# Kernel optimization log

Hardware: AMD Instinct MI355X
Metric: run time of the kernel (lower is better)

Reference implementation:

```python
import jax, jax.numpy as jnp
import numpy as np

N_NODES = 100000
N_EDGES = 3200000


def _spmm(rows, cols, vals, x):
    # out[i] = sum_{e: rows[e]==i} vals[e] * x[cols[e]]
    msgs = vals[:, None] * x[cols]  # [E, F]
    return jax.ops.segment_sum(msgs, rows, num_segments=N_NODES)


def setup_inputs() -> dict:
    key = jax.random.key(0)
    ks = jax.random.split(key, 8)
    x = jax.random.normal(ks[0], (N_NODES, 256), dtype=jnp.float32)
    adj_rows = jax.random.randint(ks[1], (N_EDGES,), 0, N_NODES, dtype=jnp.int32)
    adj_cols = jax.random.randint(ks[2], (N_EDGES,), 0, N_NODES, dtype=jnp.int32)
    adj_vals = jax.random.uniform(ks[3], (N_EDGES,), dtype=jnp.float32)
    W1 = jax.random.normal(ks[4], (256, 128), dtype=jnp.float32) * (1.0 / np.sqrt(256))
    b1 = jnp.zeros((128,), dtype=jnp.float32)
    W2 = jax.random.normal(ks[5], (128, 64), dtype=jnp.float32) * (1.0 / np.sqrt(128))
    b2 = jnp.zeros((64,), dtype=jnp.float32)
    return {"x": x, "adj_rows": adj_rows, "adj_cols": adj_cols, "adj_vals": adj_vals,
            "W1": W1, "b1": b1, "W2": W2, "b2": b2}


def reference(x, adj_rows, adj_cols, adj_vals, W1, b1, W2, b2):
    # Layer 0: spmm -> linear -> relu (dropout inactive in eval)
    h = _spmm(adj_rows, adj_cols, adj_vals, x)
    h = jax.nn.relu(h @ W1 + b1)
    # Layer 1 (last layer): spmm -> linear, no activation
    h = _spmm(adj_rows, adj_cols, adj_vals, h)
    out = h @ W2 + b2
    return out  # squeeze(1) is a no-op for [N, nclass]
```

## Files before the change

### kernel.cpp

```cpp
#include <hip/hip_runtime.h>
#include <hip/hip_fp16.h>


#define RPB 480
#define NB_MAX 1024
#define PCHUNK 8192
#define EPT 32

typedef _Float16 half8 __attribute__((ext_vector_type(8)));
typedef float floatx4 __attribute__((ext_vector_type(4)));

__global__ __launch_bounds__(256) void zero_i32_kernel(int* __restrict__ p, int n) {
    int i = blockIdx.x * 256 + threadIdx.x;
    if (i < n) p[i] = 0;
}

__global__ __launch_bounds__(256) void transpose_w_kernel(const float* __restrict__ W,
                                                          __half* __restrict__ WT,
                                                          int K, int N) {
    int i = blockIdx.x * 256 + threadIdx.x;
    if (i < K * N) {
        int k = i / N, n = i % N;
        WT[n * K + k] = __float2half_rn(W[i]);
    }
}

__global__ __launch_bounds__(256) void bucket_hist_kernel(const int* __restrict__ rows,
                                                          int* __restrict__ gcnt,
                                                          int nE, int nB) {
    __shared__ int hist[NB_MAX];
    const int t = threadIdx.x;
    const int c0 = blockIdx.x * PCHUNK;
    const int c1 = min(c0 + PCHUNK, nE);
    for (int b = t; b < nB; b += 256) hist[b] = 0;
    __syncthreads();
    for (int e = c0 + t; e < c1; e += 256) atomicAdd(&hist[rows[e] / RPB], 1);
    __syncthreads();
    for (int b = t; b < nB; b += 256) {
        int c = hist[b];
        if (c) atomicAdd(&gcnt[b], c);
    }
}

__global__ __launch_bounds__(1024) void bucket_scan_kernel(const int* __restrict__ gcnt,
                                                           int* __restrict__ boff,
                                                           int* __restrict__ gcur,
                                                           int* __restrict__ off,
                                                           int nB, int nN) {
    __shared__ int part[1024];
    int t = threadIdx.x;
    int v = (t < nB) ? gcnt[t] : 0;
    part[t] = v;
    __syncthreads();
    for (int d = 1; d < 1024; d <<= 1) {
        int add = (t >= d) ? part[t - d] : 0;
        __syncthreads();
        part[t] += add;
        __syncthreads();
    }
    if (t < nB) {
        int excl = part[t] - v;
        boff[t] = excl;
        gcur[t] = excl;
    }
    if (t == 1023) {
        boff[nB] = part[1023];
        off[nN] = part[1023];
    }
}

__global__ __launch_bounds__(256) void partition_kernel(const int* __restrict__ rows,
                                                        const int* __restrict__ cols,
                                                        const float* __restrict__ vals,
                                                        int* __restrict__ gcur,
                                                        int2* __restrict__ eb1,
                                                        int nE, int nB) {
    __shared__ int hist[NB_MAX];
    __shared__ int cur[NB_MAX];
    const int t = threadIdx.x;
    const int c0 = blockIdx.x * PCHUNK;
    for (int b = t; b < nB; b += 256) hist[b] = 0;
    __syncthreads();
    int myr[EPT];
#pragma unroll
    for (int j = 0; j < EPT; ++j) {
        int e = c0 + t + 256 * j;
        int r = (e < nE) ? rows[e] : -1;
        myr[j] = r;
        if (r >= 0) atomicAdd(&hist[r / RPB], 1);
    }
    __syncthreads();
    for (int b = t; b < nB; b += 256) {
        int c = hist[b];
        cur[b] = c ? atomicAdd(&gcur[b], c) : 0;
    }
    __syncthreads();
#pragma unroll
    for (int j = 0; j < EPT; ++j) {
        int r = myr[j];
        if (r >= 0) {
            int e = c0 + t + 256 * j;
            int bk = r / RPB;
            int rl = r - bk * RPB;
            int pos = atomicAdd(&cur[bk], 1);
            eb1[pos] = make_int2((cols[e] & 0x1FFFF) | (rl << 17), __float_as_int(vals[e]));
        }
    }
}

__global__ __launch_bounds__(512) void fine_scatter_kernel(const int* __restrict__ boff,
                                                           const int2* __restrict__ eb1,
                                                           int2* __restrict__ eb2,
                                                           int* __restrict__ off,
                                                           int nN) {
    __shared__ int hist[RPB];
    __shared__ int sc[RPB];
    __shared__ int cur[RPB];
    const int b = blockIdx.x;
    const int row0 = b * RPB;
    const int nr = min(RPB, nN - row0);
    const int t = threadIdx.x;
    const int s = boff[b];
    const int e = boff[b + 1];

    if (t < RPB) hist[t] = 0;
    __syncthreads();
    for (int i = s + t; i < e; i += 512)
        atomicAdd(&hist[((unsigned)eb1[i].x) >> 17], 1);
    __syncthreads();

    int myc = (t < RPB) ? hist[t] : 0;
    if (t < RPB) sc[t] = myc;
    __syncthreads();
    for (int d = 1; d < RPB; d <<= 1) {
        int add = (t < RPB && t >= d) ? sc[t - d] : 0;
        __syncthreads();
        if (t < RPB) sc[t] += add;
        __syncthreads();
    }
    if (t < RPB) {
        int excl = s + sc[t] - myc;
        cur[t] = excl;
        if (t < nr) off[row0 + t] = excl;
    }
    __syncthreads();

    for (int i = s + t; i < e; i += 512) {
        int2 ed = eb1[i];
        unsigned x = (unsigned)ed.x;
        int pos = atomicAdd(&cur[x >> 17], 1);
        eb2[pos] = make_int2((int)(x & 0x1FFFF), ed.y);
    }
}

template <int F>
__global__ __launch_bounds__(256) void spmm_csr_kernel(const int* __restrict__ off,
                                                       const int2* __restrict__ eb,
                                                       const __half* __restrict__ Y,
                                                       const float* __restrict__ bias,
                                                       float* __restrict__ out, int nN) {
    int row = blockIdx.x * 4 + (threadIdx.x >> 6);
    if (row >= nN) return;
    int lane = threadIdx.x & 63;
    int s = off[row];
    int e1 = off[row + 1];

    float2 acc;
    if (F == 128) acc = make_float2(bias[lane * 2], bias[lane * 2 + 1]);
    else          acc = make_float2(bias[lane], 0.f);

    for (int base = s; base < e1; base += 64) {
        int n = min(64, e1 - base);
        int2 my = (lane < n) ? eb[base + lane] : make_int2(0, 0);
        int j = 0;
        for (; j + 4 <= n; j += 4) {
            int c0 = __shfl(my.x, j + 0), c1 = __shfl(my.x, j + 1);
            int c2 = __shfl(my.x, j + 2), c3 = __shfl(my.x, j + 3);
            float v0 = __int_as_float(__shfl(my.y, j + 0));
            float v1 = __int_as_float(__shfl(my.y, j + 1));
            float v2 = __int_as_float(__shfl(my.y, j + 2));
            float v3 = __int_as_float(__shfl(my.y, j + 3));
            if (F == 128) {
                float2 y0 = __half22float2(*((const __half2*)(Y + (size_t)c0 * 128) + lane));
                float2 y1 = __half22float2(*((const __half2*)(Y + (size_t)c1 * 128) + lane));
                float2 y2 = __half22float2(*((const __half2*)(Y + (size_t)c2 * 128) + lane));
                float2 y3 = __half22float2(*((const __half2*)(Y + (size_t)c3 * 128) + lane));
                acc.x = fmaf(v0, y0.x, acc.x); acc.y = fmaf(v0, y0.y, acc.y);
                acc.x = fmaf(v1, y1.x, acc.x); acc.y = fmaf(v1, y1.y, acc.y);
                acc.x = fmaf(v2, y2.x, acc.x); acc.y = fmaf(v2, y2.y, acc.y);
                acc.x = fmaf(v3, y3.x, acc.x); acc.y = fmaf(v3, y3.y, acc.y);
            } else {
                float y0 = __half2float(Y[(size_t)c0 * 64 + lane]);
                float y1 = __half2float(Y[(size_t)c1 * 64 + lane]);
                float y2 = __half2float(Y[(size_t)c2 * 64 + lane]);
                float y3 = __half2float(Y[(size_t)c3 * 64 + lane]);
                acc.x = fmaf(v0, y0, acc.x);
                acc.x = fmaf(v1, y1, acc.x);
                acc.x = fmaf(v2, y2, acc.x);
                acc.x = fmaf(v3, y3, acc.x);
            }
        }
        for (; j < n; ++j) {
            int c = __shfl(my.x, j);
            float v = __int_as_float(__shfl(my.y, j));
            if (F == 128) {
                float2 y = __half22float2(*((const __half2*)(Y + (size_t)c * 128) + lane));
                acc.x = fmaf(v, y.x, acc.x);
                acc.y = fmaf(v, y.y, acc.y);
            } else {
                acc.x = fmaf(v, __half2float(Y[(size_t)c * 64 + lane]), acc.x);
            }
        }
    }

    if (F == 128) {
        *(float2*)(out + (size_t)row * 128 + lane * 2) = acc;
    } else {
        out[(size_t)row * 64 + lane] = acc.x;
    }
}

__global__ __launch_bounds__(256) void init_bias_kernel(float* __restrict__ out,
                                                        const float* __restrict__ bias,
                                                        int fmask, size_t total) {
    size_t i = (size_t)blockIdx.x * 256 + threadIdx.x;
    if (i < total) out[i] = bias[i & fmask];
}

template <int F>
__global__ __launch_bounds__(256) void spmm_atomic_kernel(const int* __restrict__ rows,
                                                          const int* __restrict__ cols,
                                                          const float* __restrict__ vals,
                                                          const __half* __restrict__ Y,
                                                          float* __restrict__ out, int nE) {
    int e = blockIdx.x * 4 + (threadIdx.x >> 6);
    if (e >= nE) return;
    int lane = threadIdx.x & 63;
    int r = rows[e];
    int c = cols[e];
    float v = vals[e];
    if (F == 128) {
        float2 y = __half22float2(*((const __half2*)(Y + (size_t)c * 128) + lane));
        float* op = out + (size_t)r * 128 + lane * 2;
        unsafeAtomicAdd(op, v * y.x);
        unsafeAtomicAdd(op + 1, v * y.y);
    } else {
        float y = __half2float(Y[(size_t)c * F + lane]);
        unsafeAtomicAdd(out + (size_t)r * F + lane, v * y);
    }
}

template <int NN, int KK, bool RELU_IN>
__global__ __launch_bounds__(256) void gemm_mfma_kernel(const float* __restrict__ A,
                                                        const __half* __restrict__ BT,
                                                        __half* __restrict__ C, int nrows) {
    constexpr int MT = 64, KT = 64, KP = KT + 8;
    __shared__ __half As[MT * KP];
    __shared__ __half Bs[NN * KP];
    const int tid = threadIdx.x;
    const int wid = tid >> 6, lane = tid & 63;
    const int row0 = blockIdx.x * MT;
    const int wr = wid & 1, wc = wid >> 1;
    constexpr int WCT = NN / 32;
    const int lrow = lane & 15, q = lane >> 4;

    floatx4 acc[2][WCT];
#pragma unroll
    for (int rt = 0; rt < 2; ++rt)
#pragma unroll
        for (int ct = 0; ct < WCT; ++ct)
#pragma unroll
            for (int i = 0; i < 4; ++i) acc[rt][ct][i] = 0.f;

    for (int kt = 0; kt < KK; kt += KT) {
#pragma unroll
        for (int it = 0; it < MT * KT / 4 / 256; ++it) {
            int i4 = it * 256 + tid;
            int m = i4 >> 4;
            int kk = (i4 & 15) << 2;
            int gr = row0 + m;
            float4 v = make_float4(0.f, 0.f, 0.f, 0.f);
            if (gr < nrows) v = *(const float4*)(A + (size_t)gr * KK + kt + kk);
            if (RELU_IN) {
                v.x = fmaxf(v.x, 0.f); v.y = fmaxf(v.y, 0.f);
                v.z = fmaxf(v.z, 0.f); v.w = fmaxf(v.w, 0.f);
            }
            __half h0 = __float2half_rn(v.x), h1 = __float2half_rn(v.y);
            __half h2 = __float2half_rn(v.z), h3 = __float2half_rn(v.w);
            ushort4 u = make_ushort4(*(unsigned short*)&h0, *(unsigned short*)&h1,
                                     *(unsigned short*)&h2, *(unsigned short*)&h3);
            *(ushort4*)(As + m * KP + kk) = u;
        }
#pragma unroll
        for (int it = 0; it < NN * KT / 4 / 256; ++it) {
            int i4 = it * 256 + tid;
            int n = i4 >> 4;
            int kk = (i4 & 15) << 2;
            *(ushort4*)(Bs + n * KP + kk) =
                *(const ushort4*)(BT + (size_t)n * KK + kt + kk);
        }
        __syncthreads();

#pragma unroll
        for (int ks = 0; ks < KT; ks += 32) {
            half8 a0 = *(half8*)(As + (wr * 32 + lrow) * KP + ks + q * 8);
            half8 a1 = *(half8*)(As + (wr * 32 + 16 + lrow) * KP + ks + q * 8);
#pragma unroll
            for (int ct = 0; ct < WCT; ++ct) {
                half8 b = *(half8*)(Bs + (wc * (NN / 2) + ct * 16 + lrow) * KP + ks + q * 8);
                acc[0][ct] = __builtin_amdgcn_mfma_f32_16x16x32_f16(a0, b, acc[0][ct], 0, 0, 0);
                acc[1][ct] = __builtin_amdgcn_mfma_f32_16x16x32_f16(a1, b, acc[1][ct], 0, 0, 0);
            }
        }
        __syncthreads();
    }

#pragma unroll
    for (int rt = 0; rt < 2; ++rt)
#pragma unroll
        for (int ct = 0; ct < WCT; ++ct)
#pragma unroll
            for (int r = 0; r < 4; ++r) {
                int gr = row0 + wr * 32 + rt * 16 + q * 4 + r;
                if (gr < nrows)
                    C[(size_t)gr * NN + wc * (NN / 2) + ct * 16 + lrow] =
                        __float2half_rn(acc[rt][ct][r]);
            }
}

extern "C" void kernel_launch(void* const* d_in, const int* in_sizes, int n_in,
                              void* d_out, int out_size, void* d_ws, size_t ws_size,
                              hipStream_t stream) {
    const float* x    = (const float*)d_in[0];
    const int*   rows = (const int*)d_in[1];
    const int*   cols = (const int*)d_in[2];
    const float* vals = (const float*)d_in[3];
    const float* W1   = (const float*)d_in[4];
    const float* b1   = (const float*)d_in[5];
    const float* W2   = (const float*)d_in[6];
    const float* b2   = (const float*)d_in[7];
    float* out = (float*)d_out;

    const int nN = in_sizes[0] / 256;
    const int nE = in_sizes[1];
    const int nB = (nN + RPB - 1) / RPB;

    char* w = (char*)d_ws;
    __half* Y1h = (__half*)w;   w += (size_t)nN * 128 * 2;
    float*  H1  = (float*)w;    w += (size_t)nN * 128 * 4;
    __half* Y2h = Y1h;
    __half* W1T = (__half*)w;   w += (size_t)256 * 128 * 2;
    __half* W2T = (__half*)w;   w += (size_t)128 * 64 * 2;
    int*  off   = (int*)w;      w += ((size_t)nN + 4) * 4;
    int*  gcnt  = (int*)w;      w += (size_t)NB_MAX * 4;
    int*  boff  = (int*)w;      w += (size_t)(NB_MAX + 4) * 4;
    int*  gcur  = (int*)w;      w += (size_t)NB_MAX * 4;
    int2* eb1   = (int2*)w;     w += (size_t)nE * 8;
    int2* eb2   = (int2*)w;     w += (size_t)nE * 8;
    size_t need = (size_t)(w - (char*)d_ws);

    const int mblocks  = (nN + 63) / 64;
    const int pblocks  = (nE + PCHUNK - 1) / PCHUNK;
    const int rblocks  = (nN + 3) / 4;
    const int eblocks4 = (nE + 3) / 4;

    transpose_w_kernel<<<(256 * 128 + 255) / 256, 256, 0, stream>>>(W1, W1T, 256, 128);
    transpose_w_kernel<<<(128 * 64 + 255) / 256, 256, 0, stream>>>(W2, W2T, 128, 64);

    gemm_mfma_kernel<128, 256, false><<<mblocks, 256, 0, stream>>>(x, W1T, Y1h, nN);

    if (ws_size >= need && nN <= (1 << 17) && nB <= NB_MAX) {
        zero_i32_kernel<<<(nB + 255) / 256, 256, 0, stream>>>(gcnt, nB);
        bucket_hist_kernel<<<pblocks, 256, 0, stream>>>(rows, gcnt, nE, nB);
        bucket_scan_kernel<<<1, 1024, 0, stream>>>(gcnt, boff, gcur, off, nB, nN);
        partition_kernel<<<pblocks, 256, 0, stream>>>(rows, cols, vals, gcur, eb1, nE, nB);
        fine_scatter_kernel<<<nB, 512, 0, stream>>>(boff, eb1, eb2, off, nN);

        spmm_csr_kernel<128><<<rblocks, 256, 0, stream>>>(off, eb2, Y1h, b1, H1, nN);
        gemm_mfma_kernel<64, 128, true><<<mblocks, 256, 0, stream>>>(H1, W2T, Y2h, nN);
        spmm_csr_kernel<64><<<rblocks, 256, 0, stream>>>(off, eb2, Y2h, b2, out, nN);
    } else {
        size_t totH1 = (size_t)nN * 128;
        init_bias_kernel<<<(int)((totH1 + 255) / 256), 256, 0, stream>>>(H1, b1, 127, totH1);
        spmm_atomic_kernel<128><<<eblocks4, 256, 0, stream>>>(rows, cols, vals, Y1h, H1, nE);
        gemm_mfma_kernel<64, 128, true><<<mblocks, 256, 0, stream>>>(H1, W2T, Y2h, nN);
        size_t totOut = (size_t)nN * 64;
        init_bias_kernel<<<(int)((totOut + 255) / 256), 256, 0, stream>>>(out, b2, 63, totOut);
        spmm_atomic_kernel<64><<<eblocks4, 256, 0, stream>>>(rows, cols, vals, Y2h, out, nE);
    }
}
```

Before: 520.1 us.

## Fuse layer-1 SpMM with ReLU and W2 projection into one kernel

The first CSR SpMM now applies ReLU and then multiplies each row by W2 inside the same kernel, using fp16 dot2 against W2 staged in shared memory. This removes the fp32 H1 write/read round trip and the separate second GEMM launch. The two weight transposes are also merged into one prep kernel. The cost is that every block loads 16 KB of W2 into LDS, the per-row matvec is serial over 64 steps per wave, and H1 is rounded to fp16 before the projection.

```diff
diff --git a/kernel.cpp b/kernel.cpp
--- a/kernel.cpp
+++ b/kernel.cpp
@@ -8,11 +8,32 @@
 #define EPT 32
 
 typedef _Float16 half8 __attribute__((ext_vector_type(8)));
+typedef _Float16 h2t __attribute__((ext_vector_type(2)));
 typedef float floatx4 __attribute__((ext_vector_type(4)));
 
 __global__ __launch_bounds__(256) void zero_i32_kernel(int* __restrict__ p, int n) {
     int i = blockIdx.x * 256 + threadIdx.x;
     if (i < n) p[i] = 0;
+}
+
+__global__ __launch_bounds__(256) void prep_weights_kernel(const float* __restrict__ W1,
+                                                           const float* __restrict__ W2,
+                                                           __half* __restrict__ W1T,
+                                                           h2t* __restrict__ pk) {
+    int i = blockIdx.x * 256 + threadIdx.x;
+    if (i < 256 * 128) {
+        int k = i >> 7, n = i & 127;
+        W1T[n * 256 + k] = __float2half_rn(W1[i]);
+    } else {
+        int j = i - 256 * 128;
+        if (j < 4096) {
+            int kk = j >> 6, c = j & 63;
+            h2t v;
+            v[0] = (_Float16)W2[(2 * kk) * 64 + c];
+            v[1] = (_Float16)W2[(2 * kk + 1) * 64 + c];
+            pk[j] = v;
+        }
+    }
 }
 
 __global__ __launch_bounds__(256) void transpose_w_kernel(const float* __restrict__ W,
@@ -153,22 +174,88 @@
     }
 }
 
-template <int F>
-__global__ __launch_bounds__(256) void spmm_csr_kernel(const int* __restrict__ off,
-                                                       const int2* __restrict__ eb,
-                                                       const __half* __restrict__ Y,
-                                                       const float* __restrict__ bias,
-                                                       float* __restrict__ out, int nN) {
+__global__ __launch_bounds__(256) void spmm_fused_kernel(const int* __restrict__ off,
+                                                         const int2* __restrict__ eb,
+                                                         const __half* __restrict__ Y,
+                                                         const float* __restrict__ b1,
+                                                         const h2t* __restrict__ pk,
+                                                         __half* __restrict__ Y2, int nN) {
+    __shared__ h2t w2s[64 * 64];
+    __shared__ h2t hs[4][64];
+    const int t = threadIdx.x;
+#pragma unroll
+    for (int i = 0; i < 16; ++i) w2s[i * 256 + t] = pk[i * 256 + t];
+    __syncthreads();
+
+    const int row = blockIdx.x * 4 + (t >> 6);
+    const int wv = t >> 6;
+    const int lane = t & 63;
+
+    if (row < nN) {
+        float2 acc = make_float2(b1[lane * 2], b1[lane * 2 + 1]);
+        int s = off[row];
+        int e1 = off[row + 1];
+        for (int base = s; base < e1; base += 64) {
+            int n = min(64, e1 - base);
+            int2 my = (lane < n) ? eb[base + lane] : make_int2(0, 0);
+            int j = 0;
+            for (; j + 4 <= n; j += 4) {
+                int c0 = __shfl(my.x, j + 0), c1 = __shfl(my.x, j + 1);
+                int c2 = __shfl(my.x, j + 2), c3 = __shfl(my.x, j + 3);
+                float v0 = __int_as_float(__shfl(my.y, j + 0));
+                float v1 = __int_as_float(__shfl(my.y, j + 1));
+                float v2 = __int_as_float(__shfl(my.y, j + 2));
+                float v3 = __int_as_float(__shfl(my.y, j + 3));
+                float2 y0 = __half22float2(*((const __half2*)(Y + (size_t)c0 * 128) + lane));
+                float2 y1 = __half22float2(*((const __half2*)(Y + (size_t)c1 * 128) + lane));
+                float2 y2 = __half22float2(*((const __half2*)(Y + (size_t)c2 * 128) + lane));
+                float2 y3 = __half22float2(*((const __half2*)(Y + (size_t)c3 * 128) + lane));
+                acc.x = fmaf(v0, y0.x, acc.x); acc.y = fmaf(v0, y0.y, acc.y);
+                acc.x = fmaf(v1, y1.x, acc.x); acc.y = fmaf(v1, y1.y, acc.y);
+                acc.x = fmaf(v2, y2.x, acc.x); acc.y = fmaf(v2, y2.y, acc.y);
+                acc.x = fmaf(v3, y3.x, acc.x); acc.y = fmaf(v3, y3.y, acc.y);
+            }
+            for (; j < n; ++j) {
+                int c = __shfl(my.x, j);
+                float v = __int_as_float(__shfl(my.y, j));
+                float2 y = __half22float2(*((const __half2*)(Y + (size_t)c * 128) + lane));
+                acc.x = fmaf(v, y.x, acc.x);
+                acc.y = fmaf(v, y.y, acc.y);
+            }
+        }
+        h2t hv;
+        hv[0] = (_Float16)fmaxf(acc.x, 0.f);
+        hv[1] = (_Float16)fmaxf(acc.y, 0.f);
+        hs[wv][lane] = hv;
+
+        float o = 0.f;
+#pragma unroll 8
+        for (int kk = 0; kk < 64; ++kk) {
+            h2t a = hs[wv][kk];
+            h2t b = w2s[kk * 64 + lane];
+#if __has_builtin(__builtin_amdgcn_fdot2)
+            o = __builtin_amdgcn_fdot2(a, b, o, false);
+#else
+            o = fmaf((float)a[0], (float)b[0], o);
+            o = fmaf((float)a[1], (float)b[1], o);
+#endif
+        }
+        Y2[(size_t)row * 64 + lane] = __float2half_rn(o);
+    }
+}
+
+__global__ __launch_bounds__(256) void spmm_csr64_kernel(const int* __restrict__ off,
+                                                         const int2* __restrict__ eb,
+                                                         const __half* __restrict__ Y,
+                                                         const float* __restrict__ bias,
+                                                         float* __restrict__ out, int nN) {
     int row = blockIdx.x * 4 + (threadIdx.x >> 6);
     if (row >= nN) return;
     int lane = threadIdx.x & 63;
     int s = off[row];
     int e1 = off[row + 1];
 
-    float2 acc;
-    if (F == 128) acc = make_float2(bias[lane * 2], bias[lane * 2 + 1]);
-    else          acc = make_float2(bias[lane], 0.f);
-
+    float acc = bias[lane];
     for (int base = s; base < e1; base += 64) {
         int n = min(64, e1 - base);
         int2 my = (lane < n) ? eb[base + lane] : make_int2(0, 0);
@@ -180,44 +267,22 @@
             float v1 = __int_as_float(__shfl(my.y, j + 1));
             float v2 = __int_as_float(__shfl(my.y, j + 2));
             float v3 = __int_as_float(__shfl(my.y, j + 3));
-            if (F == 128) {
-                float2 y0 = __half22float2(*((const __half2*)(Y + (size_t)c0 * 128) + lane));
-                float2 y1 = __half22float2(*((const __half2*)(Y + (size_t)c1 * 128) + lane));
-                float2 y2 = __half22float2(*((const __half2*)(Y + (size_t)c2 * 128) + lane));
-                float2 y3 = __half22float2(*((const __half2*)(Y + (size_t)c3 * 128) + lane));
-                acc.x = fmaf(v0, y0.x, acc.x); acc.y = fmaf(v0, y0.y, acc.y);
-                acc.x = fmaf(v1, y1.x, acc.x); acc.y = fmaf(v1, y1.y, acc.y);
-                acc.x = fmaf(v2, y2.x, acc.x); acc.y = fmaf(v2, y2.y, acc.y);
-                acc.x = fmaf(v3, y3.x, acc.x); acc.y = fmaf(v3, y3.y, acc.y);
-            } else {
-                float y0 = __half2float(Y[(size_t)c0 * 64 + lane]);
-                float y1 = __half2float(Y[(size_t)c1 * 64 + lane]);
-                float y2 = __half2float(Y[(size_t)c2 * 64 + lane]);
-                float y3 = __half2float(Y[(size_t)c3 * 64 + lane]);
-                acc.x = fmaf(v0, y0, acc.x);
-                acc.x = fmaf(v1, y1, acc.x);
-                acc.x = fmaf(v2, y2, acc.x);
-                acc.x = fmaf(v3, y3, acc.x);
-            }
+            float y0 = __half2float(Y[(size_t)c0 * 64 + lane]);
+            float y1 = __half2float(Y[(size_t)c1 * 64 + lane]);
+            float y2 = __half2float(Y[(size_t)c2 * 64 + lane]);
+            float y3 = __half2float(Y[(size_t)c3 * 64 + lane]);
+            acc = fmaf(v0, y0, acc);
+            acc = fmaf(v1, y1, acc);
+            acc = fmaf(v2, y2, acc);
+            acc = fmaf(v3, y3, acc);
         }
         for (; j < n; ++j) {
             int c = __shfl(my.x, j);
             float v = __int_as_float(__shfl(my.y, j));
-            if (F == 128) {
-                float2 y = __half22float2(*((const __half2*)(Y + (size_t)c * 128) + lane));
-                acc.x = fmaf(v, y.x, acc.x);
-                acc.y = fmaf(v, y.y, acc.y);
-            } else {
-                acc.x = fmaf(v, __half2float(Y[(size_t)c * 64 + lane]), acc.x);
-            }
-        }
-    }
-
-    if (F == 128) {
-        *(float2*)(out + (size_t)row * 128 + lane * 2) = acc;
-    } else {
-        out[(size_t)row * 64 + lane] = acc.x;
-    }
+            acc = fmaf(v, __half2float(Y[(size_t)c * 64 + lane]), acc);
+        }
+    }
+    out[(size_t)row * 64 + lane] = acc;
 }
 
 __global__ __launch_bounds__(256) void init_bias_kernel(float* __restrict__ out,
@@ -348,9 +413,10 @@
     char* w = (char*)d_ws;
     __half* Y1h = (__half*)w;   w += (size_t)nN * 128 * 2;
     float*  H1  = (float*)w;    w += (size_t)nN * 128 * 4;
-    __half* Y2h = Y1h;
+    __half* Y2h = (__half*)H1;
     __half* W1T = (__half*)w;   w += (size_t)256 * 128 * 2;
     __half* W2T = (__half*)w;   w += (size_t)128 * 64 * 2;
+    h2t*    pk  = (h2t*)w;      w += (size_t)4096 * 4;
     int*  off   = (int*)w;      w += ((size_t)nN + 4) * 4;
     int*  gcnt  = (int*)w;      w += (size_t)NB_MAX * 4;
     int*  boff  = (int*)w;      w += (size_t)(NB_MAX + 4) * 4;
@@ -364,28 +430,28 @@
     const int rblocks  = (nN + 3) / 4;
     const int eblocks4 = (nE + 3) / 4;
 
-    transpose_w_kernel<<<(256 * 128 + 255) / 256, 256, 0, stream>>>(W1, W1T, 256, 128);
-    transpose_w_kernel<<<(128 * 64 + 255) / 256, 256, 0, stream>>>(W2, W2T, 128, 64);
-
-    gemm_mfma_kernel<128, 256, false><<<mblocks, 256, 0, stream>>>(x, W1T, Y1h, nN);
-
     if (ws_size >= need && nN <= (1 << 17) && nB <= NB_MAX) {
+        prep_weights_kernel<<<(256 * 128 + 4096 + 255) / 256, 256, 0, stream>>>(W1, W2, W1T, pk);
+        gemm_mfma_kernel<128, 256, false><<<mblocks, 256, 0, stream>>>(x, W1T, Y1h, nN);
+
         zero_i32_kernel<<<(nB + 255) / 256, 256, 0, stream>>>(gcnt, nB);
         bucket_hist_kernel<<<pblocks, 256, 0, stream>>>(rows, gcnt, nE, nB);
         bucket_scan_kernel<<<1, 1024, 0, stream>>>(gcnt, boff, gcur, off, nB, nN);
         partition_kernel<<<pblocks, 256, 0, stream>>>(rows, cols, vals, gcur, eb1, nE, nB);
         fine_scatter_kernel<<<nB, 512, 0, stream>>>(boff, eb1, eb2, off, nN);
 
-        spmm_csr_kernel<128><<<rblocks, 256, 0, stream>>>(off, eb2, Y1h, b1, H1, nN);
-        gemm_mfma_kernel<64, 128, true><<<mblocks, 256, 0, stream>>>(H1, W2T, Y2h, nN);
-        spmm_csr_kernel<64><<<rblocks, 256, 0, stream>>>(off, eb2, Y2h, b2, out, nN);
+        spmm_fused_kernel<<<rblocks, 256, 0, stream>>>(off, eb2, Y1h, b1, pk, Y2h, nN);
+        spmm_csr64_kernel<<<rblocks, 256, 0, stream>>>(off, eb2, Y2h, b2, out, nN);
     } else {
+        transpose_w_kernel<<<(256 * 128 + 255) / 256, 256, 0, stream>>>(W1, W1T, 256, 128);
+        transpose_w_kernel<<<(128 * 64 + 255) / 256, 256, 0, stream>>>(W2, W2T, 128, 64);
+        gemm_mfma_kernel<128, 256, false><<<mblocks, 256, 0, stream>>>(x, W1T, Y1h, nN);
         size_t totH1 = (size_t)nN * 128;
         init_bias_kernel<<<(int)((totH1 + 255) / 256), 256, 0, stream>>>(H1, b1, 127, totH1);
         spmm_atomic_kernel<128><<<eblocks4, 256, 0, stream>>>(rows, cols, vals, Y1h, H1, nE);
-        gemm_mfma_kernel<64, 128, true><<<mblocks, 256, 0, stream>>>(H1, W2T, Y2h, nN);
+        gemm_mfma_kernel<64, 128, true><<<mblocks, 256, 0, stream>>>(H1, W2T, Y1h, nN);
         size_t totOut = (size_t)nN * 64;
         init_bias_kernel<<<(int)((totOut + 255) / 256), 256, 0, stream>>>(out, b2, 63, totOut);
-        spmm_atomic_kernel<64><<<eblocks4, 256, 0, stream>>>(rows, cols, vals, Y2h, out, nE);
-    }
-}
+        spmm_atomic_kernel<64><<<eblocks4, 256, 0, stream>>>(rows, cols, vals, Y1h, out, nE);
+    }
+}
```

New measurement: 518.2 us. Within noise of the previous version (-0.4%).
